# Kernel optimization log

Measured on AMD Instinct MI355X. Metric: run time of the kernel, lower is better.

The kernel has to match this reference:

```python
import jax, jax.numpy as jnp
import numpy as np

B, S, D = 2, 2048, 1024
H, DK = 16, 64


def setup_inputs() -> dict:
    key = jax.random.key(0)
    ks = jax.random.split(key, 5)
    x = jax.random.normal(ks[0], (B, S, D), dtype=jnp.float32)
    attn_w = jax.random.normal(ks[1], (3 * H * DK, D), dtype=jnp.float32) * (1.0 / np.sqrt(D))
    attn_b = jax.random.normal(ks[2], (3 * H * DK,), dtype=jnp.float32) * 0.02
    proj_w = jax.random.normal(ks[3], (D, H * DK), dtype=jnp.float32) * (1.0 / np.sqrt(H * DK))
    proj_b = jax.random.normal(ks[4], (D,), dtype=jnp.float32) * 0.02
    return {"x": x, "attn_w": attn_w, "attn_b": attn_b, "proj_w": proj_w, "proj_b": proj_b}


def reference(x, attn_w, attn_b, proj_w, proj_b):
    b, s, d = x.shape
    # fused QKV projection (torch Linear: x @ W.T + b)
    qkv = x @ attn_w.T + attn_b  # [b, s, 3*H*DK]
    q, k, v = jnp.split(qkv, 3, axis=2)
    # [b, s, H, DK] -> [b, H, s, DK]
    q = q.reshape(b, s, H, DK).transpose(0, 2, 1, 3)
    k = k.reshape(b, s, H, DK).transpose(0, 2, 1, 3)
    v = v.reshape(b, s, H, DK).transpose(0, 2, 1, 3)
    scale = 1.0 / np.sqrt(DK).astype(np.float32)
    scores = jnp.einsum('bhqd,bhkd->bhqk', q, k) * scale  # [b, H, s, s]
    causal = jnp.tril(jnp.ones((s, s), dtype=bool))
    scores = jnp.where(causal, scores, jnp.finfo(scores.dtype).min)
    attn = jax.nn.softmax(scores, axis=-1)
    out = jnp.einsum('bhqk,bhkd->bhqd', attn, v)  # [b, H, s, DK]
    out = out.transpose(0, 2, 1, 3).reshape(b, s, H * DK)
    return out @ proj_w.T + proj_b
```

## Files before the change

### kernel.cpp

```cpp
#include <hip/hip_runtime.h>
#include <hip/hip_bf16.h>
#include <stdint.h>


typedef __bf16 bf16_t;
typedef __bf16 bf16x8 __attribute__((ext_vector_type(8)));
typedef float f32x4 __attribute__((ext_vector_type(4)));

#define B_SZ 2
#define S_LEN 2048
#define D_MODEL 1024
#define N_HEADS 16
#define D_HEAD 64
#define M_ROWS (B_SZ * S_LEN)
#define QKV_N (3 * N_HEADS * D_HEAD)

#define Q_SCALE 0.1803368801111204f

#define OFF_XB  (0ull)
#define OFF_WB  (8ull  << 20)
#define OFF_PWB (14ull << 20)
#define OFF_Q   (16ull << 20)
#define OFF_K   (24ull << 20)
#define OFF_VT  (32ull << 20)
#define OFF_AO  (40ull << 20)

__device__ __forceinline__ unsigned short f2bf_u(float f) {
  union { float f; unsigned u; } v; v.f = f;
  unsigned r = v.u + 0x7fffu + ((v.u >> 16) & 1u);
  return (unsigned short)(r >> 16);
}
__device__ __forceinline__ bf16_t f2bf(float f) {
  unsigned short u = f2bf_u(f);
  return __builtin_bit_cast(bf16_t, u);
}
__device__ __forceinline__ unsigned cvt_pk_bf16(float lo, float hi) {
  unsigned r;
  asm volatile("v_cvt_pk_bf16_f32 %0, %1, %2" : "=v"(r) : "v"(lo), "v"(hi));
  return r;
}

__global__ void cvt3_f32_bf16(const float* __restrict__ sa, bf16_t* __restrict__ da, int n4a,
                              const float* __restrict__ sb, bf16_t* __restrict__ db, int n4b,
                              const float* __restrict__ sc, bf16_t* __restrict__ dc, int n4c) {
  int i = blockIdx.x * blockDim.x + threadIdx.x;
  const float* s; bf16_t* d; int j = i;
  if (i < n4a) { s = sa; d = da; }
  else if ((j = i - n4a) < n4b) { s = sb; d = db; }
  else if ((j = i - n4a - n4b) < n4c) { s = sc; d = dc; }
  else return;
  float4 f = reinterpret_cast<const float4*>(s)[j];
  ushort4 o;
  o.x = f2bf_u(f.x); o.y = f2bf_u(f.y); o.z = f2bf_u(f.z); o.w = f2bf_u(f.w);
  reinterpret_cast<ushort4*>(d)[j] = o;
}

#define BM 128
#define BN 128
#define BK 64

__device__ __forceinline__ void gload_lds16(const bf16_t* g, bf16_t* l) {
  __builtin_amdgcn_global_load_lds((__attribute__((address_space(1))) void*)g,
                                   (__attribute__((address_space(3))) void*)l,
                                   16, 0, 0);
}

__device__ __forceinline__ bf16x8 lds_frag(const bf16_t* lds, int row, int kchunk) {
  int pos = kchunk ^ (row & 7);
  return *reinterpret_cast<const bf16x8*>(lds + row * BK + pos * 8);
}

template <int EPI>
__global__ __launch_bounds__(256, 3) void gemm_bt(
    const bf16_t* __restrict__ A, const bf16_t* __restrict__ Bt,
    const float* __restrict__ bias,
    float* __restrict__ fout,
    bf16_t* __restrict__ qout, bf16_t* __restrict__ kout,
    bf16_t* __restrict__ vtout,
    int M, int N, int K) {
  __shared__ __align__(16) char smem[34816];
  bf16_t* As = reinterpret_cast<bf16_t*>(smem);
  bf16_t* Bs = As + BM * BK;

  const int tid = threadIdx.x;
  const int lane = tid & 63;
  const int wid = tid >> 6;
  const int wr = wid >> 1, wc = wid & 1;
  const int cl = lane & 15, hl = lane >> 4;

  const int id = blockIdx.x;
  const int xcd = id & 7, loc = id >> 3;
  int mtile, ntile;
  if constexpr (EPI == 0) {
    mtile = (xcd & 3) * 8 + (loc & 7);
    ntile = (xcd >> 2) * 12 + (loc >> 3);
  } else {
    mtile = xcd * 4 + (loc & 3);
    ntile = loc >> 2;
  }
  const int m0 = mtile * BM, n0 = ntile * BN;

  f32x4 acc[4][4];
  #pragma unroll
  for (int m = 0; m < 4; ++m)
    #pragma unroll
    for (int n = 0; n < 4; ++n)
      acc[m][n] = (f32x4){0.f, 0.f, 0.f, 0.f};

  for (int kt = 0; kt < K; kt += BK) {
    #pragma unroll
    for (int it = 0; it < 4; ++it) {
      int chunk = it * 256 + tid;
      int row = chunk >> 3, cpos = chunk & 7;
      int csrc = cpos ^ (row & 7);
      bf16_t* ldsA = As + (it * 256 + wid * 64) * 8;
      bf16_t* ldsB = Bs + (it * 256 + wid * 64) * 8;
      gload_lds16(A  + (size_t)(m0 + row) * K + kt + csrc * 8, ldsA);
      gload_lds16(Bt + (size_t)(n0 + row) * K + kt + csrc * 8, ldsB);
    }
    __syncthreads();

    bf16x8 af[2][4], bfr[2][4];
    #pragma unroll
    for (int kk = 0; kk < 2; ++kk) {
      #pragma unroll
      for (int m = 0; m < 4; ++m)
        af[kk][m] = lds_frag(As, wr * 64 + m * 16 + cl, kk * 4 + hl);
      #pragma unroll
      for (int n = 0; n < 4; ++n)
        bfr[kk][n] = lds_frag(Bs, wc * 64 + n * 16 + cl, kk * 4 + hl);
    }
    __builtin_amdgcn_s_setprio(1);
    #pragma unroll
    for (int m = 0; m < 4; ++m)
      #pragma unroll
      for (int n = 0; n < 4; ++n) {
        acc[m][n] = __builtin_amdgcn_mfma_f32_16x16x32_bf16(af[0][m], bfr[0][n], acc[m][n], 0, 0, 0);
        acc[m][n] = __builtin_amdgcn_mfma_f32_16x16x32_bf16(af[1][m], bfr[1][n], acc[m][n], 0, 0, 0);
      }
    __builtin_amdgcn_s_setprio(0);
    __syncthreads();
  }

  if constexpr (EPI == 0) {
    const int part = n0 >> 10;
    const int b = m0 >> 11;
    const int sloc = m0 & 2047;
    if (part == 2) {
      #pragma unroll
      for (int n = 0; n < 4; ++n) {
        int ng = n0 + wc * 64 + n * 16 + cl;
        float bv = bias[ng];
        int r = ng & 1023;
        int h = r >> 6, dk = r & 63;
        bf16_t* vrow = vtout + ((size_t)((b * N_HEADS + h) * D_HEAD + dk)) * S_LEN;
        #pragma unroll
        for (int m = 0; m < 4; ++m) {
          int sbase = sloc + wr * 64 + m * 16 + hl * 4;
          uint2 u;
          u.x = cvt_pk_bf16(acc[m][n][0] + bv, acc[m][n][1] + bv);
          u.y = cvt_pk_bf16(acc[m][n][2] + bv, acc[m][n][3] + bv);
          *reinterpret_cast<uint2*>(vrow + sbase) = u;
        }
      }
    } else {
      const float scale = (part == 0) ? Q_SCALE : 1.0f;
      bf16_t (*ct)[136] = reinterpret_cast<bf16_t(*)[136]>(smem);
      #pragma unroll
      for (int n = 0; n < 4; ++n) {
        int colb = wc * 64 + n * 16 + cl;
        float bv = bias[n0 + colb];
        #pragma unroll
        for (int m = 0; m < 4; ++m)
          #pragma unroll
          for (int j = 0; j < 4; ++j) {
            int row = wr * 64 + m * 16 + hl * 4 + j;
            ct[row][colb] = f2bf((acc[m][n][j] + bv) * scale);
          }
      }
      __syncthreads();
      bf16_t* dst = (part == 0) ? qout : kout;
      const int row = tid >> 1, seg = tid & 1;
      const int ngs = n0 + seg * 64;
      const int h = (ngs & 1023) >> 6;
      const int s = sloc + row;
      bf16_t* drow = dst + ((size_t)((b * N_HEADS + h) * S_LEN + s)) * D_HEAD;
      #pragma unroll
      for (int kk = 0; kk < 8; ++kk) {
        uint4 v = *reinterpret_cast<const uint4*>(&ct[row][seg * 64 + kk * 8]);
        *reinterpret_cast<uint4*>(drow + kk * 8) = v;
      }
    }
  } else {
    float (*ctf)[68] = reinterpret_cast<float(*)[68]>(smem);
    #pragma unroll 1
    for (int p = 0; p < 2; ++p) {
      if (wc == p) {
        #pragma unroll
        for (int n = 0; n < 4; ++n) {
          int coll = n * 16 + cl;
          float bv = bias[n0 + p * 64 + coll];
          #pragma unroll
          for (int m = 0; m < 4; ++m)
            #pragma unroll
            for (int j = 0; j < 4; ++j) {
              int row = wr * 64 + m * 16 + hl * 4 + j;
              ctf[row][coll] = acc[m][n][j] + bv;
            }
        }
      }
      __syncthreads();
      {
        const int row = tid >> 1, sub = tid & 1;
        float* drow = fout + (size_t)(m0 + row) * N + n0 + p * 64 + sub * 32;
        #pragma unroll
        for (int kk = 0; kk < 8; ++kk) {
          float4 v = *reinterpret_cast<const float4*>(&ctf[row][sub * 32 + kk * 4]);
          *reinterpret_cast<float4*>(drow + kk * 4) = v;
        }
      }
      __syncthreads();
    }
  }
}

__global__ __launch_bounds__(512, 2) void attn_fwd(
    const bf16_t* __restrict__ q,
    const bf16_t* __restrict__ k,
    const bf16_t* __restrict__ vt,
    bf16_t* __restrict__ ao) {
  const int blk = blockIdx.x;
  const int half = blk >> 8;
  const int low = blk & 255;
  const int bh = (low & 7) * 4 + ((low >> 3) & 3);
  const int qp = low >> 5;
  const int qt = half ? (15 - qp) : qp;
  const int tid = threadIdx.x;
  const int lane = tid & 63, w = tid >> 6;
  const int cl = lane & 15, hl = lane >> 4;
  const bf16_t* qb = q + (size_t)bh * S_LEN * D_HEAD;
  const bf16_t* kb = k + (size_t)bh * S_LEN * D_HEAD;
  const bf16_t* vb = vt + (size_t)bh * D_HEAD * S_LEN;
  const int b = bh >> 4, h = bh & 15;

  __shared__ bf16_t kvbuf[2][2][4096];
  __shared__ bf16_t plds[8][16][72];

  const int srow = tid >> 3;
  const int scc = (tid & 7) ^ (srow & 7);
  const int sw = cl & 7;

  const int row0 = qt * 128 + w * 16;
  const int ktb = 2 * qt + 1;

  const bf16_t* qr = qb + (size_t)(row0 + cl) * D_HEAD + hl * 8;
  bf16x8 qf0 = *reinterpret_cast<const bf16x8*>(qr);
  bf16x8 qf1 = *reinterpret_cast<const bf16x8*>(qr + 32);

  float mrow = -1e30f, lrow = 0.f;
  f32x4 acco[4];
  #pragma unroll
  for (int db = 0; db < 4; ++db) acco[db] = (f32x4){0.f, 0.f, 0.f, 0.f};

  gload_lds16(kb + (size_t)srow * D_HEAD + scc * 8, &kvbuf[0][0][w << 9]);
  gload_lds16(vb + (size_t)srow * S_LEN + scc * 8,  &kvbuf[0][1][w << 9]);
  __syncthreads();

  int cur = 0;
  for (int kt = 0; kt <= ktb; ++kt) {
    if (kt < ktb) {
      gload_lds16(kb + (size_t)((kt + 1) * 64 + srow) * D_HEAD + scc * 8,
                  &kvbuf[cur ^ 1][0][w << 9]);
      gload_lds16(vb + (size_t)srow * S_LEN + (kt + 1) * 64 + scc * 8,
                  &kvbuf[cur ^ 1][1][w << 9]);
    }

    const bool act = (kt * 64) <= (row0 + 15);
    if (act) {
      const bf16_t* kB = kvbuf[cur][0];
      const bf16_t* vB = kvbuf[cur][1];
      bf16x8 kf[4][2], vf[4][2];
      #pragma unroll
      for (int nb = 0; nb < 4; ++nb) {
        const bf16_t* kr = kB + (nb * 16 + cl) * 64;
        kf[nb][0] = *reinterpret_cast<const bf16x8*>(kr + ((hl ^ sw) << 3));
        kf[nb][1] = *reinterpret_cast<const bf16x8*>(kr + (((hl + 4) ^ sw) << 3));
      }
      #pragma unroll
      for (int db = 0; db < 4; ++db) {
        const bf16_t* vr = vB + (db * 16 + cl) * 64;
        vf[db][0] = *reinterpret_cast<const bf16x8*>(vr + ((hl ^ sw) << 3));
        vf[db][1] = *reinterpret_cast<const bf16x8*>(vr + (((hl + 4) ^ sw) << 3));
      }

      f32x4 sacc[4];
      __builtin_amdgcn_s_setprio(1);
      #pragma unroll
      for (int nb = 0; nb < 4; ++nb) {
        f32x4 s = (f32x4){0.f, 0.f, 0.f, 0.f};
        s = __builtin_amdgcn_mfma_f32_16x16x32_bf16(kf[nb][0], qf0, s, 0, 0, 0);
        s = __builtin_amdgcn_mfma_f32_16x16x32_bf16(kf[nb][1], qf1, s, 0, 0, 0);
        sacc[nb] = s;
      }
      __builtin_amdgcn_s_setprio(0);

      const int qrow = row0 + cl;
      if (kt * 64 + 63 > qrow) {
        #pragma unroll
        for (int nb = 0; nb < 4; ++nb)
          #pragma unroll
          for (int jj = 0; jj < 4; ++jj) {
            int kpos = kt * 64 + nb * 16 + hl * 4 + jj;
            if (kpos > qrow) sacc[nb][jj] = -1e30f;
          }
      }
      float tm = sacc[0][0];
      #pragma unroll
      for (int nb = 0; nb < 4; ++nb)
        #pragma unroll
        for (int jj = 0; jj < 4; ++jj)
          tm = fmaxf(tm, sacc[nb][jj]);
      tm = fmaxf(tm, __shfl_xor(tm, 16));
      tm = fmaxf(tm, __shfl_xor(tm, 32));
      if (__any(tm > mrow + 8.f)) {
        float mnew = fmaxf(mrow, tm);
        float corr = __builtin_amdgcn_exp2f(mrow - mnew);
        mrow = mnew;
        lrow *= corr;
        #pragma unroll
        for (int db = 0; db < 4; ++db) acco[db] *= corr;
      }
      float rs = 0.f;
      #pragma unroll
      for (int nb = 0; nb < 4; ++nb)
        #pragma unroll
        for (int jj = 0; jj < 4; ++jj) {
          float p = __builtin_amdgcn_exp2f(sacc[nb][jj] - mrow);
          sacc[nb][jj] = p;
          rs += p;
        }
      rs += __shfl_xor(rs, 16);
      rs += __shfl_xor(rs, 32);
      lrow += rs;
      #pragma unroll
      for (int nb = 0; nb < 4; ++nb) {
        uint2 u;
        u.x = cvt_pk_bf16(sacc[nb][0], sacc[nb][1]);
        u.y = cvt_pk_bf16(sacc[nb][2], sacc[nb][3]);
        *reinterpret_cast<uint2*>(&plds[w][cl][nb * 16 + hl * 4]) = u;
      }

      bf16x8 pf0 = *reinterpret_cast<const bf16x8*>(&plds[w][cl][hl * 8]);
      bf16x8 pf1 = *reinterpret_cast<const bf16x8*>(&plds[w][cl][32 + hl * 8]);
      __builtin_amdgcn_s_setprio(1);
      #pragma unroll
      for (int db = 0; db < 4; ++db) {
        acco[db] = __builtin_amdgcn_mfma_f32_16x16x32_bf16(vf[db][0], pf0, acco[db], 0, 0, 0);
        acco[db] = __builtin_amdgcn_mfma_f32_16x16x32_bf16(vf[db][1], pf1, acco[db], 0, 0, 0);
      }
      __builtin_amdgcn_s_setprio(0);
    }

    __syncthreads();
    cur ^= 1;
  }

  {
    float linv = 1.f / lrow;
    const int qrow = row0 + cl;
    #pragma unroll
    for (int db = 0; db < 4; ++db) {
      uint2 u;
      u.x = cvt_pk_bf16(acco[db][0] * linv, acco[db][1] * linv);
      u.y = cvt_pk_bf16(acco[db][2] * linv, acco[db][3] * linv);
      *reinterpret_cast<uint2*>(
          ao + ((size_t)(b * S_LEN) + qrow) * D_MODEL + h * D_HEAD + db * 16 + hl * 4) = u;
    }
  }
}

extern "C" void kernel_launch(void* const* d_in, const int* in_sizes, int n_in,
                              void* d_out, int out_size, void* d_ws, size_t ws_size,
                              hipStream_t stream) {
  const float* x      = (const float*)d_in[0];
  const float* attn_w = (const float*)d_in[1];
  const float* attn_b = (const float*)d_in[2];
  const float* proj_w = (const float*)d_in[3];
  const float* proj_b = (const float*)d_in[4];
  float* out = (float*)d_out;
  char* ws = (char*)d_ws;

  bf16_t* xb  = (bf16_t*)(ws + OFF_XB);
  bf16_t* wb  = (bf16_t*)(ws + OFF_WB);
  bf16_t* pwb = (bf16_t*)(ws + OFF_PWB);
  bf16_t* qb  = (bf16_t*)(ws + OFF_Q);
  bf16_t* kb  = (bf16_t*)(ws + OFF_K);
  bf16_t* vtb = (bf16_t*)(ws + OFF_VT);
  bf16_t* aob = (bf16_t*)(ws + OFF_AO);

  const int n4a = M_ROWS * D_MODEL / 4;
  const int n4b = QKV_N * D_MODEL / 4;
  const int n4c = D_MODEL * D_MODEL / 4;
  const int n4 = n4a + n4b + n4c;
  cvt3_f32_bf16<<<(n4 + 255) / 256, 256, 0, stream>>>(x, xb, n4a, attn_w, wb, n4b,
                                                      proj_w, pwb, n4c);

  gemm_bt<0><<<dim3(768), 256, 0, stream>>>(
      xb, wb, attn_b, nullptr, qb, kb, vtb, M_ROWS, QKV_N, D_MODEL);

  attn_fwd<<<dim3(512), 512, 0, stream>>>(qb, kb, vtb, aob);

  gemm_bt<1><<<dim3(256), 256, 0, stream>>>(
      aob, pwb, proj_b, out, nullptr, nullptr, nullptr, M_ROWS, D_MODEL, D_MODEL);
}
```

Baseline: 116.4 us.

## Replace QKV GEMM with 256x256 double-buffered tile kernel

```diff
diff --git a/kernel.cpp b/kernel.cpp
--- a/kernel.cpp
+++ b/kernel.cpp
@@ -55,28 +55,119 @@
   reinterpret_cast<ushort4*>(d)[j] = o;
 }
 
-#define BM 128
-#define BN 128
-#define BK 64
-
 __device__ __forceinline__ void gload_lds16(const bf16_t* g, bf16_t* l) {
   __builtin_amdgcn_global_load_lds((__attribute__((address_space(1))) void*)g,
                                    (__attribute__((address_space(3))) void*)l,
                                    16, 0, 0);
 }
 
+__global__ __launch_bounds__(512, 1) void gemm256_qkv(
+    const bf16_t* __restrict__ A, const bf16_t* __restrict__ Bt,
+    const float* __restrict__ bias,
+    bf16_t* __restrict__ qout, bf16_t* __restrict__ kout,
+    bf16_t* __restrict__ vtout, int K) {
+  __shared__ bf16_t As[2][16384];
+  __shared__ bf16_t Bs[2][16384];
+  const int tid = threadIdx.x;
+  const int lane = tid & 63, wid = tid >> 6;
+  const int wr = wid >> 2, wc = wid & 3;
+  const int cl = lane & 15, hl = lane >> 4;
+  const int id = blockIdx.x;
+  const int m0 = (id & 15) * 256, n0 = (id >> 4) * 256;
+
+  f32x4 acc[8][4];
+  #pragma unroll
+  for (int m = 0; m < 8; ++m)
+    #pragma unroll
+    for (int n = 0; n < 4; ++n)
+      acc[m][n] = (f32x4){0.f, 0.f, 0.f, 0.f};
+
+  #define STAGE256(buf, kt)                                                     \
+    {                                                                           \
+      _Pragma("unroll")                                                         \
+      for (int it = 0; it < 4; ++it) {                                          \
+        int c = it * 512 + tid;                                                 \
+        int row = c >> 3, cpos = c & 7;                                         \
+        int csrc = cpos ^ (row & 7);                                            \
+        gload_lds16(A  + (size_t)(m0 + row) * K + (kt) + csrc * 8,              \
+                    &As[buf][(it * 512 + wid * 64) * 8]);                       \
+        gload_lds16(Bt + (size_t)(n0 + row) * K + (kt) + csrc * 8,              \
+                    &Bs[buf][(it * 512 + wid * 64) * 8]);                       \
+      }                                                                         \
+    }
+
+  STAGE256(0, 0);
+  __syncthreads();
+
+  int cur = 0;
+  for (int kt = 0; kt < K; kt += 64) {
+    if (kt + 64 < K) STAGE256(cur ^ 1, kt + 64);
+
+    #pragma unroll
+    for (int kk = 0; kk < 2; ++kk) {
+      bf16x8 af[8], bfr[4];
+      #pragma unroll
+      for (int m = 0; m < 8; ++m) {
+        int row = wr * 128 + m * 16 + cl;
+        af[m] = *reinterpret_cast<const bf16x8*>(
+            &As[cur][row * 64 + (((kk * 4 + hl) ^ (row & 7)) << 3)]);
+      }
+      #pragma unroll
+      for (int n = 0; n < 4; ++n) {
+        int row = wc * 64 + n * 16 + cl;
+        bfr[n] = *reinterpret_cast<const bf16x8*>(
+            &Bs[cur][row * 64 + (((kk * 4 + hl) ^ (row & 7)) << 3)]);
+      }
+      __builtin_amdgcn_s_setprio(1);
+      #pragma unroll
+      for (int m = 0; m < 8; ++m)
+        #pragma unroll
+        for (int n = 0; n < 4; ++n)
+          acc[m][n] = __builtin_amdgcn_mfma_f32_16x16x32_bf16(af[m], bfr[n], acc[m][n], 0, 0, 0);
+      __builtin_amdgcn_s_setprio(0);
+    }
+    __syncthreads();
+    cur ^= 1;
+  }
+  #undef STAGE256
+
+  #pragma unroll
+  for (int n = 0; n < 4; ++n) {
+    int ng = n0 + wc * 64 + n * 16 + cl;
+    float bv = bias[ng];
+    int part = ng >> 10;
+    int r = ng & 1023;
+    int h = r >> 6, dk = r & 63;
+    #pragma unroll
+    for (int m = 0; m < 8; ++m)
+      #pragma unroll
+      for (int j = 0; j < 4; ++j) {
+        int mg = m0 + wr * 128 + m * 16 + hl * 4 + j;
+        int b = mg >> 11, s = mg & 2047;
+        float val = acc[m][n][j] + bv;
+        size_t bh = (size_t)(b * N_HEADS + h);
+        if (part == 0)
+          qout[(bh * S_LEN + s) * D_HEAD + dk] = f2bf(val * Q_SCALE);
+        else if (part == 1)
+          kout[(bh * S_LEN + s) * D_HEAD + dk] = f2bf(val);
+        else
+          vtout[(bh * D_HEAD + dk) * S_LEN + s] = f2bf(val);
+      }
+  }
+}
+
+#define BM 128
+#define BN 128
+#define BK 64
+
 __device__ __forceinline__ bf16x8 lds_frag(const bf16_t* lds, int row, int kchunk) {
   int pos = kchunk ^ (row & 7);
   return *reinterpret_cast<const bf16x8*>(lds + row * BK + pos * 8);
 }
 
-template <int EPI>
-__global__ __launch_bounds__(256, 3) void gemm_bt(
+__global__ __launch_bounds__(256, 3) void gemm_proj(
     const bf16_t* __restrict__ A, const bf16_t* __restrict__ Bt,
-    const float* __restrict__ bias,
-    float* __restrict__ fout,
-    bf16_t* __restrict__ qout, bf16_t* __restrict__ kout,
-    bf16_t* __restrict__ vtout,
+    const float* __restrict__ bias, float* __restrict__ fout,
     int M, int N, int K) {
   __shared__ __align__(16) char smem[34816];
   bf16_t* As = reinterpret_cast<bf16_t*>(smem);
@@ -90,14 +181,8 @@
 
   const int id = blockIdx.x;
   const int xcd = id & 7, loc = id >> 3;
-  int mtile, ntile;
-  if constexpr (EPI == 0) {
-    mtile = (xcd & 3) * 8 + (loc & 7);
-    ntile = (xcd >> 2) * 12 + (loc >> 3);
-  } else {
-    mtile = xcd * 4 + (loc & 3);
-    ntile = loc >> 2;
-  }
+  const int mtile = xcd * 4 + (loc & 3);
+  const int ntile = loc >> 2;
   const int m0 = mtile * BM, n0 = ntile * BN;
 
   f32x4 acc[4][4];
@@ -113,10 +198,10 @@
       int chunk = it * 256 + tid;
       int row = chunk >> 3, cpos = chunk & 7;
       int csrc = cpos ^ (row & 7);
-      bf16_t* ldsA = As + (it * 256 + wid * 64) * 8;
-      bf16_t* ldsB = Bs + (it * 256 + wid * 64) * 8;
-      gload_lds16(A  + (size_t)(m0 + row) * K + kt + csrc * 8, ldsA);
-      gload_lds16(Bt + (size_t)(n0 + row) * K + kt + csrc * 8, ldsB);
+      gload_lds16(A  + (size_t)(m0 + row) * K + kt + csrc * 8,
+                  As + (it * 256 + wid * 64) * 8);
+      gload_lds16(Bt + (size_t)(n0 + row) * K + kt + csrc * 8,
+                  Bs + (it * 256 + wid * 64) * 8);
     }
     __syncthreads();
 
@@ -142,85 +227,34 @@
     __syncthreads();
   }
 
-  if constexpr (EPI == 0) {
-    const int part = n0 >> 10;
-    const int b = m0 >> 11;
-    const int sloc = m0 & 2047;
-    if (part == 2) {
+  float (*ctf)[68] = reinterpret_cast<float(*)[68]>(smem);
+  #pragma unroll 1
+  for (int p = 0; p < 2; ++p) {
+    if (wc == p) {
       #pragma unroll
       for (int n = 0; n < 4; ++n) {
-        int ng = n0 + wc * 64 + n * 16 + cl;
-        float bv = bias[ng];
-        int r = ng & 1023;
-        int h = r >> 6, dk = r & 63;
-        bf16_t* vrow = vtout + ((size_t)((b * N_HEADS + h) * D_HEAD + dk)) * S_LEN;
-        #pragma unroll
-        for (int m = 0; m < 4; ++m) {
-          int sbase = sloc + wr * 64 + m * 16 + hl * 4;
-          uint2 u;
-          u.x = cvt_pk_bf16(acc[m][n][0] + bv, acc[m][n][1] + bv);
-          u.y = cvt_pk_bf16(acc[m][n][2] + bv, acc[m][n][3] + bv);
-          *reinterpret_cast<uint2*>(vrow + sbase) = u;
-        }
-      }
-    } else {
-      const float scale = (part == 0) ? Q_SCALE : 1.0f;
-      bf16_t (*ct)[136] = reinterpret_cast<bf16_t(*)[136]>(smem);
-      #pragma unroll
-      for (int n = 0; n < 4; ++n) {
-        int colb = wc * 64 + n * 16 + cl;
-        float bv = bias[n0 + colb];
+        int coll = n * 16 + cl;
+        float bv = bias[n0 + p * 64 + coll];
         #pragma unroll
         for (int m = 0; m < 4; ++m)
           #pragma unroll
           for (int j = 0; j < 4; ++j) {
             int row = wr * 64 + m * 16 + hl * 4 + j;
-            ct[row][colb] = f2bf((acc[m][n][j] + bv) * scale);
+            ctf[row][coll] = acc[m][n][j] + bv;
           }
       }
-      __syncthreads();
-      bf16_t* dst = (part == 0) ? qout : kout;
-      const int row = tid >> 1, seg = tid & 1;
-      const int ngs = n0 + seg * 64;
-      const int h = (ngs & 1023) >> 6;
-      const int s = sloc + row;
-      bf16_t* drow = dst + ((size_t)((b * N_HEADS + h) * S_LEN + s)) * D_HEAD;
+    }
+    __syncthreads();
+    {
+      const int row = tid >> 1, sub = tid & 1;
+      float* drow = fout + (size_t)(m0 + row) * N + n0 + p * 64 + sub * 32;
       #pragma unroll
       for (int kk = 0; kk < 8; ++kk) {
-        uint4 v = *reinterpret_cast<const uint4*>(&ct[row][seg * 64 + kk * 8]);
-        *reinterpret_cast<uint4*>(drow + kk * 8) = v;
-      }
-    }
-  } else {
-    float (*ctf)[68] = reinterpret_cast<float(*)[68]>(smem);
-    #pragma unroll 1
-    for (int p = 0; p < 2; ++p) {
-      if (wc == p) {
-        #pragma unroll
-        for (int n = 0; n < 4; ++n) {
-          int coll = n * 16 + cl;
-          float bv = bias[n0 + p * 64 + coll];
-          #pragma unroll
-          for (int m = 0; m < 4; ++m)
-            #pragma unroll
-            for (int j = 0; j < 4; ++j) {
-              int row = wr * 64 + m * 16 + hl * 4 + j;
-              ctf[row][coll] = acc[m][n][j] + bv;
-            }
-        }
-      }
-      __syncthreads();
-      {
-        const int row = tid >> 1, sub = tid & 1;
-        float* drow = fout + (size_t)(m0 + row) * N + n0 + p * 64 + sub * 32;
-        #pragma unroll
-        for (int kk = 0; kk < 8; ++kk) {
-          float4 v = *reinterpret_cast<const float4*>(&ctf[row][sub * 32 + kk * 4]);
-          *reinterpret_cast<float4*>(drow + kk * 4) = v;
-        }
-      }
-      __syncthreads();
-    }
+        float4 v = *reinterpret_cast<const float4*>(&ctf[row][sub * 32 + kk * 4]);
+        *reinterpret_cast<float4*>(drow + kk * 4) = v;
+      }
+    }
+    __syncthreads();
   }
 }
 
@@ -405,11 +439,10 @@
   cvt3_f32_bf16<<<(n4 + 255) / 256, 256, 0, stream>>>(x, xb, n4a, attn_w, wb, n4b,
                                                       proj_w, pwb, n4c);
 
-  gemm_bt<0><<<dim3(768), 256, 0, stream>>>(
-      xb, wb, attn_b, nullptr, qb, kb, vtb, M_ROWS, QKV_N, D_MODEL);
+  gemm256_qkv<<<dim3(192), 512, 0, stream>>>(xb, wb, attn_b, qb, kb, vtb, D_MODEL);
 
   attn_fwd<<<dim3(512), 512, 0, stream>>>(qb, kb, vtb, aob);
 
-  gemm_bt<1><<<dim3(256), 256, 0, stream>>>(
-      aob, pwb, proj_b, out, nullptr, nullptr, nullptr, M_ROWS, D_MODEL, D_MODEL);
-}
+  gemm_proj<<<dim3(256), 256, 0, stream>>>(aob, pwb, proj_b, out,
+                                           M_ROWS, D_MODEL, D_MODEL);
+}
```

Result: slower. 141.6 us (+21.7%).

## Keep softmax probabilities in registers by permuting V fragment loads

Applied to the files above, without the earlier changes.

```diff
diff --git a/kernel.cpp b/kernel.cpp
--- a/kernel.cpp
+++ b/kernel.cpp
@@ -244,7 +244,6 @@
   const int b = bh >> 4, h = bh & 15;
 
   __shared__ bf16_t kvbuf[2][2][4096];
-  __shared__ bf16_t plds[8][16][72];
 
   const int srow = tid >> 3;
   const int scc = (tid & 7) ^ (srow & 7);
@@ -256,6 +255,12 @@
   const bf16_t* qr = qb + (size_t)(row0 + cl) * D_HEAD + hl * 8;
   bf16x8 qf0 = *reinterpret_cast<const bf16x8*>(qr);
   bf16x8 qf1 = *reinterpret_cast<const bf16x8*>(qr + 32);
+
+  const int co = (hl & 1) << 2;
+  const int c0 = (((hl >> 1) + 0) ^ sw) << 3;
+  const int c1 = (((hl >> 1) + 2) ^ sw) << 3;
+  const int c2 = (((hl >> 1) + 4) ^ sw) << 3;
+  const int c3 = (((hl >> 1) + 6) ^ sw) << 3;
 
   float mrow = -1e30f, lrow = 0.f;
   f32x4 acco[4];
@@ -279,18 +284,25 @@
     if (act) {
       const bf16_t* kB = kvbuf[cur][0];
       const bf16_t* vB = kvbuf[cur][1];
-      bf16x8 kf[4][2], vf[4][2];
+      bf16x8 kf[4][2];
       #pragma unroll
       for (int nb = 0; nb < 4; ++nb) {
         const bf16_t* kr = kB + (nb * 16 + cl) * 64;
         kf[nb][0] = *reinterpret_cast<const bf16x8*>(kr + ((hl ^ sw) << 3));
         kf[nb][1] = *reinterpret_cast<const bf16x8*>(kr + (((hl + 4) ^ sw) << 3));
       }
+      bf16x8 vf[4][2];
       #pragma unroll
       for (int db = 0; db < 4; ++db) {
         const bf16_t* vr = vB + (db * 16 + cl) * 64;
-        vf[db][0] = *reinterpret_cast<const bf16x8*>(vr + ((hl ^ sw) << 3));
-        vf[db][1] = *reinterpret_cast<const bf16x8*>(vr + (((hl + 4) ^ sw) << 3));
+        uint2 lo0 = *reinterpret_cast<const uint2*>(vr + c0 + co);
+        uint2 hi0 = *reinterpret_cast<const uint2*>(vr + c1 + co);
+        uint2 lo1 = *reinterpret_cast<const uint2*>(vr + c2 + co);
+        uint2 hi1 = *reinterpret_cast<const uint2*>(vr + c3 + co);
+        uint4 v0 = make_uint4(lo0.x, lo0.y, hi0.x, hi0.y);
+        uint4 v1 = make_uint4(lo1.x, lo1.y, hi1.x, hi1.y);
+        vf[db][0] = __builtin_bit_cast(bf16x8, v0);
+        vf[db][1] = __builtin_bit_cast(bf16x8, v1);
       }
 
       f32x4 sacc[4];
@@ -342,16 +354,20 @@
       rs += __shfl_xor(rs, 16);
       rs += __shfl_xor(rs, 32);
       lrow += rs;
-      #pragma unroll
-      for (int nb = 0; nb < 4; ++nb) {
-        uint2 u;
-        u.x = cvt_pk_bf16(sacc[nb][0], sacc[nb][1]);
-        u.y = cvt_pk_bf16(sacc[nb][2], sacc[nb][3]);
-        *reinterpret_cast<uint2*>(&plds[w][cl][nb * 16 + hl * 4]) = u;
-      }
-
-      bf16x8 pf0 = *reinterpret_cast<const bf16x8*>(&plds[w][cl][hl * 8]);
-      bf16x8 pf1 = *reinterpret_cast<const bf16x8*>(&plds[w][cl][32 + hl * 8]);
+
+      unsigned u00 = cvt_pk_bf16(sacc[0][0], sacc[0][1]);
+      unsigned u01 = cvt_pk_bf16(sacc[0][2], sacc[0][3]);
+      unsigned u10 = cvt_pk_bf16(sacc[1][0], sacc[1][1]);
+      unsigned u11 = cvt_pk_bf16(sacc[1][2], sacc[1][3]);
+      unsigned u20 = cvt_pk_bf16(sacc[2][0], sacc[2][1]);
+      unsigned u21 = cvt_pk_bf16(sacc[2][2], sacc[2][3]);
+      unsigned u30 = cvt_pk_bf16(sacc[3][0], sacc[3][1]);
+      unsigned u31 = cvt_pk_bf16(sacc[3][2], sacc[3][3]);
+      uint4 pw0 = make_uint4(u00, u01, u10, u11);
+      uint4 pw1 = make_uint4(u20, u21, u30, u31);
+      bf16x8 pf0 = __builtin_bit_cast(bf16x8, pw0);
+      bf16x8 pf1 = __builtin_bit_cast(bf16x8, pw1);
+
       __builtin_amdgcn_s_setprio(1);
       #pragma unroll
       for (int db = 0; db < 4; ++db) {
```

Result: slower. 122.0 us (+4.9%).
